# Optimization experiments

Hardware: AMD Instinct MI355X
Metric: run time of the kernel (lower is better)

## Reference

```python
import jax, jax.numpy as jnp
import numpy as np

D_MODEL = 1024
N_HEADS = 16
D_HEAD = D_MODEL // N_HEADS
D_FF = 4096
ACT_BITS = 8
GSIZE = 64
EPS = 1e-6


def act_quant(x):
    # per-group int8 activation quantization with straight-through estimator
    qmax = 2.0 ** (ACT_BITS - 1) - 1.0  # 127
    g = x.reshape(x.shape[:-1] + (-1, GSIZE))
    s = jnp.clip(jnp.max(jnp.abs(g), axis=-1, keepdims=True), 1e-5, None) / qmax
    q = jnp.clip(jnp.round(g / s), -qmax, qmax) * s
    out = g + jax.lax.stop_gradient(q - g)  # STE
    return out.reshape(x.shape)


def weight_quant_1b(w):
    # binarize to sign(w) * mean(|w|), STE
    alpha = jnp.mean(jnp.abs(w))
    wq = jnp.sign(w) * alpha
    return w + jax.lax.stop_gradient(wq - w)


def bitlinear(x, w):
    # y = Q_act(x) @ Q_w(w)^T ; w is [out, in]
    return act_quant(x) @ weight_quant_1b(w).T


def rmsnorm(x, g):
    return x * jax.lax.rsqrt(jnp.mean(x * x, axis=-1, keepdims=True) + EPS) * g


def causal_sdpa(q, k, v):
    # q,k,v: [B,H,T,Dh]
    T = q.shape[2]
    scores = jnp.einsum('bhqd,bhkd->bhqk', q, k) / jnp.sqrt(jnp.asarray(D_HEAD, q.dtype))
    mask = jnp.tril(jnp.ones((T, T), dtype=bool))
    scores = jnp.where(mask, scores, jnp.asarray(-1e30, q.dtype))
    p = jax.nn.softmax(scores, axis=-1)
    return jnp.einsum('bhqk,bhkd->bhqd', p, v)


def setup_inputs() -> dict:
    key = jax.random.key(0)
    ks = jax.random.split(key, 11)
    sd = 0.02
    inp = {
        'x': jax.random.normal(ks[0], (1, 4096, D_MODEL), dtype=jnp.float32),
        'wq': jax.random.normal(ks[1], (D_MODEL, D_MODEL), dtype=jnp.float32) * sd,
        'wk': jax.random.normal(ks[2], (D_MODEL, D_MODEL), dtype=jnp.float32) * sd,
        'wv': jax.random.normal(ks[3], (D_MODEL, D_MODEL), dtype=jnp.float32) * sd,
        'wo': jax.random.normal(ks[4], (D_MODEL, D_MODEL), dtype=jnp.float32) * sd,
        'w1': jax.random.normal(ks[5], (D_FF, D_MODEL), dtype=jnp.float32) * sd,
        'w2': jax.random.normal(ks[6], (D_FF, D_MODEL), dtype=jnp.float32) * sd,
        'w3': jax.random.normal(ks[7], (D_MODEL, D_FF), dtype=jnp.float32) * sd,
        'g1': jnp.ones((D_MODEL,), dtype=jnp.float32),
        'g2': jnp.ones((D_MODEL,), dtype=jnp.float32),
    }
    return inp


def reference(x, wq, wk, wv, wo, w1, w2, w3, g1, g2):
    B, T, C = x.shape
    # attention branch
    h = rmsnorm(x, g1)
    q = bitlinear(h, wq).reshape(B, T, N_HEADS, D_HEAD).transpose(0, 2, 1, 3)
    k = bitlinear(h, wk).reshape(B, T, N_HEADS, D_HEAD).transpose(0, 2, 1, 3)
    v = bitlinear(h, wv).reshape(B, T, N_HEADS, D_HEAD).transpose(0, 2, 1, 3)
    y = causal_sdpa(q, k, v).transpose(0, 2, 1, 3).reshape(B, T, C)
    x = x + bitlinear(y, wo)
    # SwiGLU FFN branch
    h2 = rmsnorm(x, g2)
    ff = bitlinear(jax.nn.silu(bitlinear(h2, w1)) * bitlinear(h2, w2), w3)
    return x + ff
```

## Files before the change

### kernel.cpp

```cpp
#include <hip/hip_runtime.h>
#include <math.h>


typedef unsigned short u16;
typedef __attribute__((ext_vector_type(4))) float f32x4;
typedef __attribute__((ext_vector_type(4))) unsigned short u16x4;
typedef __attribute__((ext_vector_type(8))) unsigned short u16x8;
typedef __attribute__((ext_vector_type(8))) __bf16 bf16x8;

#define DEV static __device__ __forceinline__

DEV float bf2f(u16 u) { union { unsigned i; float f; } c; c.i = ((unsigned)u) << 16; return c.f; }
DEV u16 f2bf(float f) { __bf16 b = (__bf16)f; return __builtin_bit_cast(u16, b); }
DEV float fexp2(float x) { float r; asm("v_exp_f32 %0, %1" : "=v"(r) : "v"(x)); return r; }

DEV void gload16(const void* g, void* l) {
  __builtin_amdgcn_global_load_lds((__attribute__((address_space(1))) void*)g,
                                   (__attribute__((address_space(3))) void*)l,
                                   16, 0, 0);
}

__global__ __launch_bounds__(256) void convert_sign_all(
    const float* __restrict__ w0, const float* __restrict__ w1,
    const float* __restrict__ w2, const float* __restrict__ w3,
    const float* __restrict__ w4, const float* __restrict__ w5,
    const float* __restrict__ w6, u16* __restrict__ sgn_base,
    float* __restrict__ partial) {
  __shared__ float red[4];
  const int wi = blockIdx.y;
  const float* srcs[7] = {w0, w1, w2, w3, w4, w5, w6};
  const size_t offs[7] = {0, 1048576, 2097152, 3145728, 4194304, 8388608, 12582912};
  const float* w = srcs[wi];
  u16* sgn = sgn_base + offs[wi];
  const int n4 = (wi < 4) ? 262144 : 1048576;

  float s = 0.f;
  for (int i = blockIdx.x * 256 + threadIdx.x; i < n4; i += 256 * 256) {
    f32x4 v = ((const f32x4*)w)[i];
    u16x4 o;
#pragma unroll
    for (int j = 0; j < 4; ++j) {
      float f = v[j];
      o[j] = f > 0.f ? (u16)0x3F80 : (f < 0.f ? (u16)0xBF80 : (u16)0);
      s += fabsf(f);
    }
    ((u16x4*)sgn)[i] = o;
  }
#pragma unroll
  for (int off = 32; off >= 1; off >>= 1) s += __shfl_xor(s, off);
  if ((threadIdx.x & 63) == 0) red[threadIdx.x >> 6] = s;
  __syncthreads();
  if (threadIdx.x == 0)
    partial[wi * 256 + blockIdx.x] = red[0] + red[1] + red[2] + red[3];
}

__global__ __launch_bounds__(256) void finalize_alpha(
    const float* __restrict__ partial, float* __restrict__ alphas) {
  __shared__ float red[4];
  int wi = blockIdx.x;
  float v = partial[wi * 256 + threadIdx.x];
#pragma unroll
  for (int off = 32; off >= 1; off >>= 1) v += __shfl_xor(v, off);
  if ((threadIdx.x & 63) == 0) red[threadIdx.x >> 6] = v;
  __syncthreads();
  if (threadIdx.x == 0)
    alphas[wi] = (red[0] + red[1] + red[2] + red[3]) *
                 (wi < 4 ? (1.f / 1048576.f) : (1.f / 4194304.f));
}

__global__ __launch_bounds__(256) void rmsnorm_quant(
    const float* __restrict__ x, const float* __restrict__ g, u16* __restrict__ out) {
  __shared__ float red[4];
  const int row = blockIdx.x, t = threadIdx.x;
  f32x4 v = ((const f32x4*)(x + (size_t)row * 1024))[t];
  float ss = v[0] * v[0] + v[1] * v[1] + v[2] * v[2] + v[3] * v[3];
#pragma unroll
  for (int off = 32; off >= 1; off >>= 1) ss += __shfl_xor(ss, off);
  if ((t & 63) == 0) red[t >> 6] = ss;
  __syncthreads();
  float tot = red[0] + red[1] + red[2] + red[3];
  float rinv = rsqrtf(tot * (1.f / 1024.f) + 1e-6f);
  f32x4 gg = ((const f32x4*)g)[t];
  float n[4];
#pragma unroll
  for (int j = 0; j < 4; ++j) n[j] = v[j] * rinv * gg[j];
  float gm = fmaxf(fmaxf(fabsf(n[0]), fabsf(n[1])), fmaxf(fabsf(n[2]), fabsf(n[3])));
#pragma unroll
  for (int off = 1; off <= 8; off <<= 1) gm = fmaxf(gm, __shfl_xor(gm, off));
  float s = fmaxf(gm, 1e-5f) / 127.0f;
  u16x4 o;
#pragma unroll
  for (int j = 0; j < 4; ++j) {
    float q = fminf(fmaxf(rintf(n[j] / s), -127.f), 127.f) * s;
    o[j] = f2bf(q);
  }
  ((u16x4*)out)[(size_t)row * 256 + t] = o;
}

__global__ __launch_bounds__(256) void transpose_v(
    const u16* __restrict__ qkv, u16* __restrict__ Vt) {
  __shared__ u16 T[64][65];
  const int tt = blockIdx.x, h = blockIdx.y, tid = threadIdx.x;
#pragma unroll
  for (int i = 0; i < 2; ++i) {
    int idx = i * 2048 + tid * 8;
    int trow = idx >> 6, dcol = idx & 63;
    u16x8 v = *(const u16x8*)(qkv + (size_t)(tt * 64 + trow) * 3072 + 2048 + h * 64 + dcol);
#pragma unroll
    for (int j = 0; j < 8; ++j) T[dcol + j][trow] = v[j];
  }
  __syncthreads();
#pragma unroll
  for (int i = 0; i < 2; ++i) {
    int idx = i * 2048 + tid * 8;
    int drow = idx >> 6, tcol = idx & 63;
    u16x8 v;
#pragma unroll
    for (int j = 0; j < 8; ++j) v[j] = T[drow][tcol + j];
    *(u16x8*)(Vt + ((size_t)h * 64 + drow) * 4096 + tt * 64 + tcol) = v;
  }
}

template <bool RES, int BM>
__global__ __launch_bounds__(256) void gemm_bt(
    const u16* __restrict__ A, const u16* __restrict__ B,
    const float* __restrict__ alpha, int ashift, const float* __restrict__ res,
    void* __restrict__ Cout, int M, int N, int K) {
  constexpr int NI = (BM == 128) ? 4 : 2;
  constexpr int WNE = (BM == 128) ? 64 : 32;
  __shared__ u16 As[BM * 64];
  __shared__ u16 Bs[128 * 64];
  const int tid = threadIdx.x;
  const int l = tid & 63, w = tid >> 6;
  const int wm = (BM == 128) ? (w >> 1) : 0;
  const int wn = (BM == 128) ? (w & 1) : w;
  const int lr = l & 15, lg = l >> 4;
  const int xorv = (l & 7) << 4;
  const int brow = blockIdx.y * BM;
  const int bcol = blockIdx.x * 128;
  const int src_chunk = (l & 7) ^ (l >> 3);
  const int rl = w * 8 + (l >> 3);

  f32x4 acc[4][NI];
#pragma unroll
  for (int i = 0; i < 4; ++i)
#pragma unroll
    for (int j = 0; j < NI; ++j) acc[i][j] = (f32x4){0.f, 0.f, 0.f, 0.f};

  const char* Ag = (const char*)A;
  const char* Bg = (const char*)B;
  const int nkt = K >> 6;
  for (int kt = 0; kt < nkt; ++kt) {
    __syncthreads();
    const size_t kb = (size_t)kt * 128 + src_chunk * 16;
#pragma unroll
    for (int it = 0; it < BM / 32; ++it)
      gload16(Ag + (size_t)(brow + it * 32 + rl) * (size_t)(K * 2) + kb,
              &As[(it * 32 + w * 8) * 64]);
#pragma unroll
    for (int it = 0; it < 4; ++it)
      gload16(Bg + (size_t)(bcol + it * 32 + rl) * (size_t)(K * 2) + kb,
              &Bs[(it * 32 + w * 8) * 64]);
    __syncthreads();

    bf16x8 af[4][2], bfr[NI][2];
#pragma unroll
    for (int mi = 0; mi < 4; ++mi)
#pragma unroll
      for (int ks = 0; ks < 2; ++ks) {
        int row = wm * 64 + mi * 16 + lr;
        af[mi][ks] = *(const bf16x8*)((const char*)As + row * 128 + ((ks * 64 + lg * 16) ^ xorv));
      }
#pragma unroll
    for (int ni = 0; ni < NI; ++ni)
#pragma unroll
      for (int ks = 0; ks < 2; ++ks) {
        int row = wn * WNE + ni * 16 + lr;
        bfr[ni][ks] = *(const bf16x8*)((const char*)Bs + row * 128 + ((ks * 64 + lg * 16) ^ xorv));
      }
#pragma unroll
    for (int ks = 0; ks < 2; ++ks)
#pragma unroll
      for (int mi = 0; mi < 4; ++mi)
#pragma unroll
        for (int ni = 0; ni < NI; ++ni)
          acc[mi][ni] = __builtin_amdgcn_mfma_f32_16x16x32_bf16(
              af[mi][ks], bfr[ni][ks], acc[mi][ni], 0, 0, 0);
  }

  const float scale = alpha[bcol >> ashift];
#pragma unroll
  for (int mi = 0; mi < 4; ++mi)
#pragma unroll
    for (int ni = 0; ni < NI; ++ni)
#pragma unroll
      for (int r = 0; r < 4; ++r) {
        int row = brow + wm * 64 + mi * 16 + lg * 4 + r;
        int col = bcol + wn * WNE + ni * 16 + lr;
        float vv = acc[mi][ni][r] * scale;
        if (RES)
          ((float*)Cout)[(size_t)row * N + col] = res[(size_t)row * N + col] + vv;
        else
          ((u16*)Cout)[(size_t)row * N + col] = f2bf(vv);
      }
}

__global__ __launch_bounds__(256) void gemm_ffn(
    const u16* __restrict__ A, const u16* __restrict__ B1,
    const u16* __restrict__ B2, const float* __restrict__ alpha2,
    u16* __restrict__ zq) {
  __shared__ u16 As[128 * 64];
  __shared__ u16 B1s[128 * 64];
  __shared__ u16 B2s[128 * 64];
  const int tid = threadIdx.x;
  const int l = tid & 63, w = tid >> 6;
  const int wm = w >> 1, wn = w & 1;
  const int lr = l & 15, lg = l >> 4;
  const int xorv = (l & 7) << 4;
  const int brow = blockIdx.y * 128;
  const int bcol = blockIdx.x * 128;
  const int src_chunk = (l & 7) ^ (l >> 3);
  const int rl = w * 8 + (l >> 3);
  const int K = 1024;

  f32x4 acc1[4][4], acc2[4][4];
#pragma unroll
  for (int i = 0; i < 4; ++i)
#pragma unroll
    for (int j = 0; j < 4; ++j) {
      acc1[i][j] = (f32x4){0.f, 0.f, 0.f, 0.f};
      acc2[i][j] = (f32x4){0.f, 0.f, 0.f, 0.f};
    }

  for (int kt = 0; kt < 16; ++kt) {
    __syncthreads();
    const size_t kb = (size_t)kt * 128 + src_chunk * 16;
#pragma unroll
    for (int it = 0; it < 4; ++it) {
      gload16((const char*)A + (size_t)(brow + it * 32 + rl) * 2048 + kb,
              &As[(it * 32 + w * 8) * 64]);
      gload16((const char*)B1 + (size_t)(bcol + it * 32 + rl) * 2048 + kb,
              &B1s[(it * 32 + w * 8) * 64]);
      gload16((const char*)B2 + (size_t)(bcol + it * 32 + rl) * 2048 + kb,
              &B2s[(it * 32 + w * 8) * 64]);
    }
    __syncthreads();

    bf16x8 af[4][2], bfr[4][2];
#pragma unroll
    for (int mi = 0; mi < 4; ++mi)
#pragma unroll
      for (int ks = 0; ks < 2; ++ks) {
        int row = wm * 64 + mi * 16 + lr;
        af[mi][ks] = *(const bf16x8*)((const char*)As + row * 128 + ((ks * 64 + lg * 16) ^ xorv));
      }
#pragma unroll
    for (int ni = 0; ni < 4; ++ni)
#pragma unroll
      for (int ks = 0; ks < 2; ++ks) {
        int row = wn * 64 + ni * 16 + lr;
        bfr[ni][ks] = *(const bf16x8*)((const char*)B1s + row * 128 + ((ks * 64 + lg * 16) ^ xorv));
      }
#pragma unroll
    for (int ks = 0; ks < 2; ++ks)
#pragma unroll
      for (int mi = 0; mi < 4; ++mi)
#pragma unroll
        for (int ni = 0; ni < 4; ++ni)
          acc1[mi][ni] = __builtin_amdgcn_mfma_f32_16x16x32_bf16(
              af[mi][ks], bfr[ni][ks], acc1[mi][ni], 0, 0, 0);
#pragma unroll
    for (int ni = 0; ni < 4; ++ni)
#pragma unroll
      for (int ks = 0; ks < 2; ++ks) {
        int row = wn * 64 + ni * 16 + lr;
        bfr[ni][ks] = *(const bf16x8*)((const char*)B2s + row * 128 + ((ks * 64 + lg * 16) ^ xorv));
      }
#pragma unroll
    for (int ks = 0; ks < 2; ++ks)
#pragma unroll
      for (int mi = 0; mi < 4; ++mi)
#pragma unroll
        for (int ni = 0; ni < 4; ++ni)
          acc2[mi][ni] = __builtin_amdgcn_mfma_f32_16x16x32_bf16(
              af[mi][ks], bfr[ni][ks], acc2[mi][ni], 0, 0, 0);
  }

  const float a1 = alpha2[0], a2 = alpha2[1];
  const float L2E = 1.4426950408889634f;
#pragma unroll
  for (int mi = 0; mi < 4; ++mi)
#pragma unroll
    for (int r = 0; r < 4; ++r) {
      float zz[4];
      float gm = 0.f;
#pragma unroll
      for (int ni = 0; ni < 4; ++ni) {
        float y1 = acc1[mi][ni][r] * a1;
        float y2 = acc2[mi][ni][r] * a2;
        float sg = y1 / (1.f + fexp2(-L2E * y1));
        zz[ni] = sg * y2;
        gm = fmaxf(gm, fabsf(zz[ni]));
      }
#pragma unroll
      for (int off = 1; off <= 8; off <<= 1) gm = fmaxf(gm, __shfl_xor(gm, off));
      float gmc = fmaxf(gm, 1e-5f);
      float s = gmc * (1.f / 127.f);
      float inv = 127.f / gmc;
      int row = brow + wm * 64 + mi * 16 + lg * 4 + r;
#pragma unroll
      for (int ni = 0; ni < 4; ++ni) {
        int col = bcol + wn * 64 + ni * 16 + lr;
        float q = fminf(fmaxf(rintf(zz[ni] * inv), -127.f), 127.f) * s;
        zq[(size_t)row * 4096 + col] = f2bf(q);
      }
    }
}

__global__ __launch_bounds__(256) void attn_kernel(
    const u16* __restrict__ QKV, const u16* __restrict__ Vt, u16* __restrict__ Y) {
  __shared__ u16 Ks[2][64 * 64];
  __shared__ u16 Vs[2][64 * 64];
  __shared__ u16 Ps[4][16 * 64];

  const int tid = threadIdx.x;
  const int l = tid & 63, w = tid >> 6;
  const int lr = l & 15, lg = l >> 4;
  const int xorv = (l & 7) << 4;
  const int h = blockIdx.x;
  const int y = blockIdx.y;
  const int qt = (y < 32) ? y : (95 - y);
  const int src_chunk = (l & 7) ^ (l >> 3);
  const int rl = w * 8 + (l >> 3);
  const float SC = 0.18033688f;

  const int qrow0 = qt * 64 + w * 16;
  const int nkt = qt + 1;

  bf16x8 qf[2];
#pragma unroll
  for (int ks = 0; ks < 2; ++ks)
    qf[ks] = __builtin_bit_cast(
        bf16x8, *(const u16x8*)(QKV + (size_t)(qrow0 + lr) * 3072 +
                                h * 64 + ks * 32 + lg * 8));

  f32x4 O[4];
#pragma unroll
  for (int ni = 0; ni < 4; ++ni) O[ni] = (f32x4){0.f, 0.f, 0.f, 0.f};
  float m_ = -3e38f, lsum = 0.f;

  auto STAGE = [&](int buf, int kt) {
#pragma unroll
    for (int it = 0; it < 2; ++it) {
      int krow = kt * 64 + it * 32 + rl;
      gload16((const char*)QKV + ((size_t)krow * 3072 + 1024 + h * 64) * 2 + src_chunk * 16,
              &Ks[buf][(it * 32 + w * 8) * 64]);
      int drow = it * 32 + rl;
      gload16((const char*)Vt + (((size_t)h * 64 + drow) * 4096 + kt * 64) * 2 + src_chunk * 16,
              &Vs[buf][(it * 32 + w * 8) * 64]);
    }
  };

  STAGE(0, 0);
#pragma unroll 1
  for (int kt = 0; kt < nkt; ++kt) {
    const int cur = kt & 1;
    if (kt + 1 < nkt) {
      STAGE(cur ^ 1, kt + 1);
      asm volatile("s_waitcnt vmcnt(4)" ::: "memory");
    } else {
      asm volatile("s_waitcnt vmcnt(0)" ::: "memory");
    }
    __builtin_amdgcn_s_barrier();
    __builtin_amdgcn_sched_barrier(0);

    const char* kbase = (const char*)&Ks[cur][0];
    const char* vbase = (const char*)&Vs[cur][0];

    f32x4 S[4];
    __builtin_amdgcn_s_setprio(1);
#pragma unroll
    for (int ni = 0; ni < 4; ++ni) {
      S[ni] = (f32x4){0.f, 0.f, 0.f, 0.f};
#pragma unroll
      for (int ks = 0; ks < 2; ++ks) {
        bf16x8 kf = *(const bf16x8*)(kbase + (ni * 16 + lr) * 128 +
                                     ((ks * 64 + lg * 16) ^ xorv));
        S[ni] = __builtin_amdgcn_mfma_f32_16x16x32_bf16(kf, qf[ks], S[ni], 0, 0, 0);
      }
    }
    __builtin_amdgcn_s_setprio(0);

#pragma unroll
    for (int ni = 0; ni < 4; ++ni)
#pragma unroll
      for (int r = 0; r < 4; ++r) S[ni][r] *= SC;
    if (kt == qt) {
#pragma unroll
      for (int ni = 0; ni < 4; ++ni)
#pragma unroll
        for (int r = 0; r < 4; ++r)
          if ((ni * 16 + lg * 4 + r) > (w * 16 + lr)) S[ni][r] = -3e38f;
    }

    float nm = -3e38f;
#pragma unroll
    for (int ni = 0; ni < 4; ++ni)
#pragma unroll
      for (int r = 0; r < 4; ++r) nm = fmaxf(nm, S[ni][r]);
    nm = fmaxf(nm, __shfl_xor(nm, 16));
    nm = fmaxf(nm, __shfl_xor(nm, 32));
    if (__ballot(nm > m_ + 8.f)) {
      float mn = fmaxf(m_, nm);
      float fac = fexp2(m_ - mn);
      m_ = mn;
      lsum *= fac;
#pragma unroll
      for (int ni = 0; ni < 4; ++ni) O[ni] *= fac;
    }
    float rs = 0.f;
#pragma unroll
    for (int ni = 0; ni < 4; ++ni)
#pragma unroll
      for (int r = 0; r < 4; ++r) {
        float pv = fexp2(S[ni][r] - m_);
        S[ni][r] = pv;
        rs += pv;
      }
    rs += __shfl_xor(rs, 16);
    rs += __shfl_xor(rs, 32);
    lsum += rs;

#pragma unroll
    for (int ni = 0; ni < 4; ++ni) {
      u16x4 pk;
#pragma unroll
      for (int r = 0; r < 4; ++r) pk[r] = f2bf(S[ni][r]);
      *(u16x4*)((char*)&Ps[w][0] + lr * 128 + ((ni * 32 + lg * 8) ^ xorv)) = pk;
    }
    bf16x8 pt[2];
#pragma unroll
    for (int ks = 0; ks < 2; ++ks)
      pt[ks] = *(const bf16x8*)((const char*)&Ps[w][0] + lr * 128 +
                                ((ks * 64 + lg * 16) ^ xorv));

    __builtin_amdgcn_s_setprio(1);
#pragma unroll
    for (int ni = 0; ni < 4; ++ni) {
#pragma unroll
      for (int ks = 0; ks < 2; ++ks) {
        bf16x8 vf = *(const bf16x8*)(vbase + (ni * 16 + lr) * 128 +
                                     ((ks * 64 + lg * 16) ^ xorv));
        O[ni] = __builtin_amdgcn_mfma_f32_16x16x32_bf16(vf, pt[ks], O[ni], 0, 0, 0);
      }
    }
    __builtin_amdgcn_s_setprio(0);
    asm volatile("" ::: "memory");
    __builtin_amdgcn_s_barrier();
  }

  float rinv = 1.f / lsum;
  float o[4][4];
  float gm = 0.f;
#pragma unroll
  for (int ni = 0; ni < 4; ++ni)
#pragma unroll
    for (int r = 0; r < 4; ++r) {
      o[ni][r] = O[ni][r] * rinv;
      gm = fmaxf(gm, fabsf(o[ni][r]));
    }
  gm = fmaxf(gm, __shfl_xor(gm, 16));
  gm = fmaxf(gm, __shfl_xor(gm, 32));
  float gmc = fmaxf(gm, 1e-5f);
  float s = gmc * (1.f / 127.f);
  float inv = 127.f / gmc;
#pragma unroll
  for (int ni = 0; ni < 4; ++ni) {
    u16x4 ov;
#pragma unroll
    for (int r = 0; r < 4; ++r) {
      float q = fminf(fmaxf(rintf(o[ni][r] * inv), -127.f), 127.f) * s;
      ov[r] = f2bf(q);
    }
    *(u16x4*)(Y + (size_t)(qrow0 + lr) * 1024 + h * 64 + ni * 16 + lg * 4) = ov;
  }
}

extern "C" void kernel_launch(void* const* d_in, const int* in_sizes, int n_in,
                              void* d_out, int out_size, void* d_ws, size_t ws_size,
                              hipStream_t stream) {
  const float* x  = (const float*)d_in[0];
  const float* wq = (const float*)d_in[1];
  const float* wk = (const float*)d_in[2];
  const float* wv = (const float*)d_in[3];
  const float* wo = (const float*)d_in[4];
  const float* w1 = (const float*)d_in[5];
  const float* w2 = (const float*)d_in[6];
  const float* w3 = (const float*)d_in[7];
  const float* g1 = (const float*)d_in[8];
  const float* g2 = (const float*)d_in[9];

  char* ws = (char*)d_ws;
  const size_t MB = 1024 * 1024;
  u16* sgn   = (u16*)ws;
  u16* sWq   = (u16*)(ws + 0 * MB);
  u16* sWo   = (u16*)(ws + 6 * MB);
  u16* sW1   = (u16*)(ws + 8 * MB);
  u16* sW2   = (u16*)(ws + 16 * MB);
  u16* sW3   = (u16*)(ws + 24 * MB);
  float* partial = (float*)(ws + 32 * MB);
  float* alphas  = (float*)(ws + 32 * MB + 16384);
  u16* Vt    = (u16*)(ws + 33 * MB);
  float* x1  = (float*)(ws + 33 * MB);
  u16* hq    = (u16*)(ws + 49 * MB);
  u16* qkv   = (u16*)(ws + 57 * MB);
  u16* yb    = (u16*)(ws + 81 * MB);
  u16* zq    = (u16*)(ws + 57 * MB);

  convert_sign_all<<<dim3(256, 7), 256, 0, stream>>>(wq, wk, wv, wo, w1, w2, w3,
                                                     sgn, partial);
  finalize_alpha<<<7, 256, 0, stream>>>(partial, alphas);

  rmsnorm_quant<<<4096, 256, 0, stream>>>(x, g1, hq);
  gemm_bt<false, 128><<<dim3(24, 32), 256, 0, stream>>>(hq, sWq, alphas, 10, nullptr,
                                                        qkv, 4096, 3072, 1024);
  transpose_v<<<dim3(64, 16), 256, 0, stream>>>(qkv, Vt);
  attn_kernel<<<dim3(16, 64), 256, 0, stream>>>(qkv, Vt, yb);
  gemm_bt<true, 64><<<dim3(8, 64), 256, 0, stream>>>(yb, sWo, alphas + 3, 31, x,
                                                     x1, 4096, 1024, 1024);
  rmsnorm_quant<<<4096, 256, 0, stream>>>(x1, g2, hq);
  gemm_ffn<<<dim3(32, 32), 256, 0, stream>>>(hq, sW1, sW2, alphas + 4, zq);
  gemm_bt<true, 64><<<dim3(8, 64), 256, 0, stream>>>(zq, sW3, alphas + 6, 31, x1,
                                                     (float*)d_out, 4096, 1024, 4096);
}
```

Before: 361.5 us.

## Interleave W1/W2 sign weights so FFN gate GEMM uses one B tile per block

```diff
diff --git a/kernel.cpp b/kernel.cpp
--- a/kernel.cpp
+++ b/kernel.cpp
@@ -29,10 +29,12 @@
   __shared__ float red[4];
   const int wi = blockIdx.y;
   const float* srcs[7] = {w0, w1, w2, w3, w4, w5, w6};
-  const size_t offs[7] = {0, 1048576, 2097152, 3145728, 4194304, 8388608, 12582912};
+  const size_t offs[7] = {0, 1048576, 2097152, 3145728, 4194304, 4194304, 12582912};
   const float* w = srcs[wi];
   u16* sgn = sgn_base + offs[wi];
   const int n4 = (wi < 4) ? 262144 : 1048576;
+  const bool ilv = (wi == 4) || (wi == 5);
+  const int ilv_add = (wi == 5) ? 64 : 0;
 
   float s = 0.f;
   for (int i = blockIdx.x * 256 + threadIdx.x; i < n4; i += 256 * 256) {
@@ -44,7 +46,14 @@
       o[j] = f > 0.f ? (u16)0x3F80 : (f < 0.f ? (u16)0xBF80 : (u16)0);
       s += fabsf(f);
     }
-    ((u16x4*)sgn)[i] = o;
+    size_t di = i;
+    if (ilv) {
+      int e = i << 2;
+      int row = e >> 10, col = e & 1023;
+      int dst = ((row >> 6) << 7) + ilv_add + (row & 63);
+      di = ((size_t)dst << 8) + (col >> 2);
+    }
+    ((u16x4*)sgn)[di] = o;
   }
 #pragma unroll
   for (int off = 32; off >= 1; off >>= 1) s += __shfl_xor(s, off);
@@ -206,12 +215,13 @@
 }
 
 __global__ __launch_bounds__(256) void gemm_ffn(
-    const u16* __restrict__ A, const u16* __restrict__ B1,
-    const u16* __restrict__ B2, const float* __restrict__ alpha2,
-    u16* __restrict__ zq) {
-  __shared__ u16 As[128 * 64];
-  __shared__ u16 B1s[128 * 64];
-  __shared__ u16 B2s[128 * 64];
+    const u16* __restrict__ A, const u16* __restrict__ B12,
+    const float* __restrict__ alpha2, u16* __restrict__ zq) {
+  __shared__ char smem[32768];
+  u16* As = (u16*)smem;
+  u16* Bs = (u16*)(smem + 16384);
+  float* ex = (float*)smem;
+
   const int tid = threadIdx.x;
   const int l = tid & 63, w = tid >> 6;
   const int wm = w >> 1, wn = w & 1;
@@ -221,16 +231,12 @@
   const int bcol = blockIdx.x * 128;
   const int src_chunk = (l & 7) ^ (l >> 3);
   const int rl = w * 8 + (l >> 3);
-  const int K = 1024;
-
-  f32x4 acc1[4][4], acc2[4][4];
+
+  f32x4 acc[4][4];
 #pragma unroll
   for (int i = 0; i < 4; ++i)
 #pragma unroll
-    for (int j = 0; j < 4; ++j) {
-      acc1[i][j] = (f32x4){0.f, 0.f, 0.f, 0.f};
-      acc2[i][j] = (f32x4){0.f, 0.f, 0.f, 0.f};
-    }
+    for (int j = 0; j < 4; ++j) acc[i][j] = (f32x4){0.f, 0.f, 0.f, 0.f};
 
   for (int kt = 0; kt < 16; ++kt) {
     __syncthreads();
@@ -239,10 +245,8 @@
     for (int it = 0; it < 4; ++it) {
       gload16((const char*)A + (size_t)(brow + it * 32 + rl) * 2048 + kb,
               &As[(it * 32 + w * 8) * 64]);
-      gload16((const char*)B1 + (size_t)(bcol + it * 32 + rl) * 2048 + kb,
-              &B1s[(it * 32 + w * 8) * 64]);
-      gload16((const char*)B2 + (size_t)(bcol + it * 32 + rl) * 2048 + kb,
-              &B2s[(it * 32 + w * 8) * 64]);
+      gload16((const char*)B12 + (size_t)(bcol + it * 32 + rl) * 2048 + kb,
+              &Bs[(it * 32 + w * 8) * 64]);
     }
     __syncthreads();
 
@@ -259,7 +263,7 @@
 #pragma unroll
       for (int ks = 0; ks < 2; ++ks) {
         int row = wn * 64 + ni * 16 + lr;
-        bfr[ni][ks] = *(const bf16x8*)((const char*)B1s + row * 128 + ((ks * 64 + lg * 16) ^ xorv));
+        bfr[ni][ks] = *(const bf16x8*)((const char*)Bs + row * 128 + ((ks * 64 + lg * 16) ^ xorv));
       }
 #pragma unroll
     for (int ks = 0; ks < 2; ++ks)
@@ -267,54 +271,63 @@
       for (int mi = 0; mi < 4; ++mi)
 #pragma unroll
         for (int ni = 0; ni < 4; ++ni)
-          acc1[mi][ni] = __builtin_amdgcn_mfma_f32_16x16x32_bf16(
-              af[mi][ks], bfr[ni][ks], acc1[mi][ni], 0, 0, 0);
-#pragma unroll
-    for (int ni = 0; ni < 4; ++ni)
-#pragma unroll
-      for (int ks = 0; ks < 2; ++ks) {
-        int row = wn * 64 + ni * 16 + lr;
-        bfr[ni][ks] = *(const bf16x8*)((const char*)B2s + row * 128 + ((ks * 64 + lg * 16) ^ xorv));
-      }
-#pragma unroll
-    for (int ks = 0; ks < 2; ++ks)
-#pragma unroll
-      for (int mi = 0; mi < 4; ++mi)
-#pragma unroll
-        for (int ni = 0; ni < 4; ++ni)
-          acc2[mi][ni] = __builtin_amdgcn_mfma_f32_16x16x32_bf16(
-              af[mi][ks], bfr[ni][ks], acc2[mi][ni], 0, 0, 0);
+          acc[mi][ni] = __builtin_amdgcn_mfma_f32_16x16x32_bf16(
+              af[mi][ks], bfr[ni][ks], acc[mi][ni], 0, 0, 0);
   }
 
   const float a1 = alpha2[0], a2 = alpha2[1];
   const float L2E = 1.4426950408889634f;
-#pragma unroll
-  for (int mi = 0; mi < 4; ++mi)
-#pragma unroll
-    for (int r = 0; r < 4; ++r) {
-      float zz[4];
-      float gm = 0.f;
+  __syncthreads();
+  if (wn == 1) {
+#pragma unroll
+    for (int mi = 0; mi < 4; ++mi)
 #pragma unroll
       for (int ni = 0; ni < 4; ++ni) {
-        float y1 = acc1[mi][ni][r] * a1;
-        float y2 = acc2[mi][ni][r] * a2;
-        float sg = y1 / (1.f + fexp2(-L2E * y1));
-        zz[ni] = sg * y2;
-        gm = fmaxf(gm, fabsf(zz[ni]));
-      }
-#pragma unroll
-      for (int off = 1; off <= 8; off <<= 1) gm = fmaxf(gm, __shfl_xor(gm, off));
-      float gmc = fmaxf(gm, 1e-5f);
-      float s = gmc * (1.f / 127.f);
-      float inv = 127.f / gmc;
-      int row = brow + wm * 64 + mi * 16 + lg * 4 + r;
+        int col = ni * 16 + lr;
+        int row0 = wm * 64 + mi * 16 + lg * 4;
+        int rs = row0 ^ ((col & 3) << 3);
+        f32x4 t = acc[mi][ni];
+        t[0] *= a2; t[1] *= a2; t[2] *= a2; t[3] *= a2;
+        *(f32x4*)&ex[col * 128 + rs] = t;
+      }
+  }
+  __syncthreads();
+  if (wn == 0) {
+#pragma unroll
+    for (int mi = 0; mi < 4; ++mi) {
+      f32x4 y2v[4];
 #pragma unroll
       for (int ni = 0; ni < 4; ++ni) {
-        int col = bcol + wn * 64 + ni * 16 + lr;
-        float q = fminf(fmaxf(rintf(zz[ni] * inv), -127.f), 127.f) * s;
-        zq[(size_t)row * 4096 + col] = f2bf(q);
-      }
-    }
+        int col = ni * 16 + lr;
+        int row0 = wm * 64 + mi * 16 + lg * 4;
+        y2v[ni] = *(const f32x4*)&ex[col * 128 + (row0 ^ ((col & 3) << 3))];
+      }
+#pragma unroll
+      for (int r = 0; r < 4; ++r) {
+        float zz[4];
+        float gm = 0.f;
+#pragma unroll
+        for (int ni = 0; ni < 4; ++ni) {
+          float y1 = acc[mi][ni][r] * a1;
+          float sg = y1 / (1.f + fexp2(-L2E * y1));
+          zz[ni] = sg * y2v[ni][r];
+          gm = fmaxf(gm, fabsf(zz[ni]));
+        }
+#pragma unroll
+        for (int off = 1; off <= 8; off <<= 1) gm = fmaxf(gm, __shfl_xor(gm, off));
+        float gmc = fmaxf(gm, 1e-5f);
+        float s = gmc * (1.f / 127.f);
+        float inv = 127.f / gmc;
+        int row = brow + wm * 64 + mi * 16 + lg * 4 + r;
+#pragma unroll
+        for (int ni = 0; ni < 4; ++ni) {
+          int col = blockIdx.x * 64 + ni * 16 + lr;
+          float q = fminf(fmaxf(rintf(zz[ni] * inv), -127.f), 127.f) * s;
+          zq[(size_t)row * 4096 + col] = f2bf(q);
+        }
+      }
+    }
+  }
 }
 
 __global__ __launch_bounds__(256) void attn_kernel(
@@ -505,8 +518,7 @@
   u16* sgn   = (u16*)ws;
   u16* sWq   = (u16*)(ws + 0 * MB);
   u16* sWo   = (u16*)(ws + 6 * MB);
-  u16* sW1   = (u16*)(ws + 8 * MB);
-  u16* sW2   = (u16*)(ws + 16 * MB);
+  u16* sW12  = (u16*)(ws + 8 * MB);
   u16* sW3   = (u16*)(ws + 24 * MB);
   float* partial = (float*)(ws + 32 * MB);
   float* alphas  = (float*)(ws + 32 * MB + 16384);
@@ -529,7 +541,7 @@
   gemm_bt<true, 64><<<dim3(8, 64), 256, 0, stream>>>(yb, sWo, alphas + 3, 31, x,
                                                      x1, 4096, 1024, 1024);
   rmsnorm_quant<<<4096, 256, 0, stream>>>(x1, g2, hq);
-  gemm_ffn<<<dim3(32, 32), 256, 0, stream>>>(hq, sW1, sW2, alphas + 4, zq);
+  gemm_ffn<<<dim3(64, 32), 256, 0, stream>>>(hq, sW12, alphas + 4, zq);
   gemm_bt<true, 64><<<dim3(8, 64), 256, 0, stream>>>(zq, sW3, alphas + 6, 31, x1,
                                                      (float*)d_out, 4096, 1024, 4096);
 }
```

New measurement: 339.2 us. 1.07x faster.
